# Kernel optimization log

Hardware: AMD Instinct MI355X
Metric: run time of the kernel (lower is better)

Reference implementation:

```python
import jax, jax.numpy as jnp
import numpy as np

T_SEG = 8      # n_segment
K_SIZE = 3     # dynamic temporal kernel size
BN_EPS = 1e-5


def setup_inputs() -> dict:
    key = jax.random.key(0)
    ks = jax.random.split(key, 8)
    B, T, C, H, W = 8, T_SEG, 256, 56, 56
    ch = C // 4          # c_hidden (reduction=4)
    th = T * 2           # t_hidden (temporal_expand=2)
    K = K_SIZE
    f32 = jnp.float32
    return {
        "x": jax.random.normal(ks[0], (B * T, C, H, W), f32),
        "w_spatial": jax.random.normal(ks[1], (1, 2, 7, 7), f32) * 0.05,   # Conv2d(2,1,7)
        "w_reduce": jax.random.normal(ks[2], (ch, C, 3, 1, 1), f32) * 0.02, # Conv3d(C,ch,(3,1,1))
        "bn_gamma": jnp.ones((ch,), f32),
        "bn_beta": jnp.zeros((ch,), f32),
        "bn_mean": jnp.zeros((ch,), f32),
        "bn_var": jnp.ones((ch,), f32),
        "w_expand": jax.random.normal(ks[3], (C, ch, 1, 1, 1), f32) * 0.02, # Conv3d(ch,C,1)
        "w_fc1": jax.random.normal(ks[4], (th, T), f32) * 0.1,
        "b_fc1": jnp.zeros((th,), f32),
        "w_fc2": jax.random.normal(ks[5], (K, th), f32) * 0.1,
        "b_fc2": jnp.zeros((K,), f32).at[K // 2].set(5.0),
    }


def reference(x, w_spatial, w_reduce, bn_gamma, bn_beta, bn_mean, bn_var,
              w_expand, w_fc1, b_fc1, w_fc2, b_fc2):
    T, K = T_SEG, K_SIZE
    BT, C, H, W = x.shape
    B = BT // T

    # ---- spatial SE gate: channel max/mean -> 7x7 conv -> sigmoid ----
    max_c = x.max(axis=1, keepdims=True)                       # (BT,1,H,W)
    avg_c = x.mean(axis=1, keepdims=True)                      # (BT,1,H,W)
    s = jax.lax.conv_general_dilated(
        jnp.concatenate([max_c, avg_c], axis=1), w_spatial,
        window_strides=(1, 1), padding=((3, 3), (3, 3)),
        dimension_numbers=("NCHW", "OIHW", "NCHW"))
    x_s = x * (1.0 + jax.nn.sigmoid(s))                        # (BT,C,H,W)

    # ---- temporal SE gate: conv3d(3,1,1) -> BN -> relu -> 1x1x1 -> sigmoid ----
    x5 = x_s.reshape(B, T, C, H, W).transpose(0, 2, 1, 3, 4)   # (B,C,T,H,W)
    t = jax.lax.conv_general_dilated(
        x5, w_reduce, window_strides=(1, 1, 1),
        padding=((1, 1), (0, 0), (0, 0)),
        dimension_numbers=("NCDHW", "OIDHW", "NCDHW"))         # (B,ch,T,H,W)
    inv = bn_gamma / jnp.sqrt(bn_var + BN_EPS)
    t = jax.nn.relu(t * inv[None, :, None, None, None]
                    + (bn_beta - bn_mean * inv)[None, :, None, None, None])
    t_attn = jax.nn.sigmoid(
        jnp.einsum("oc,bcthw->bothw", w_expand[:, :, 0, 0, 0], t))
    x_t = x5 * (1.0 + t_attn)                                  # (B,C,T,H,W)

    # ---- dynamic per-(batch,channel) temporal kernel ----
    v = x_t.mean(axis=(-2, -1))                                # (B,C,T)
    h = jax.nn.relu(jnp.einsum("bct,ht->bch", v, w_fc1) + b_fc1)
    kernel = jax.nn.softmax(jnp.einsum("bch,kh->bck", h, w_fc2) + b_fc2,
                            axis=-1)                           # (B,C,K)

    # depthwise temporal stencil (groups=B*C conv2d in torch)
    pad = K // 2
    xp = jnp.pad(x_t, ((0, 0), (0, 0), (pad, pad), (0, 0), (0, 0)))
    out = sum(kernel[:, :, k, None, None, None] * xp[:, :, k:k + T]
              for k in range(K))                               # (B,C,T,H,W)

    return out.transpose(0, 2, 1, 3, 4).reshape(BT, C, H, W)
```

## Files before the change

### kernel.cpp

```cpp
#include <hip/hip_runtime.h>
#include <stdint.h>

#define HW 3136
#define Wd 56
#define Cc 256
#define CH 64
#define Tt 8
#define Bb 8
#define VP 49

typedef unsigned short ushort_t;
typedef __attribute__((ext_vector_type(2))) unsigned short us2;
typedef __attribute__((ext_vector_type(4))) unsigned short us4;
typedef __attribute__((ext_vector_type(8))) unsigned short us8;
typedef __attribute__((ext_vector_type(8))) short short8;
typedef __attribute__((ext_vector_type(4))) float f4;
typedef __attribute__((ext_vector_type(2))) float f2;

__device__ __forceinline__ float bf2f(ushort_t u) {
    union { unsigned int i; float f; } v;
    v.i = ((unsigned int)u) << 16;
    return v.f;
}
__device__ __forceinline__ ushort_t f2bf(float f) {
    union { float f; unsigned int i; } v;
    v.f = f;
    unsigned int r = (v.i + 0x7FFFu + ((v.i >> 16) & 1u)) >> 16;
    return (ushort_t)r;
}

__global__ __launch_bounds__(256) void k0_pack(
    const float* __restrict__ wr, const float* __restrict__ bng,
    const float* __restrict__ bnb, const float* __restrict__ bnm,
    const float* __restrict__ bnv, const float* __restrict__ we,
    ushort_t* __restrict__ wpack, ushort_t* __restrict__ wepack,
    float* __restrict__ shb) {
    int bx = blockIdx.x, tid = threadIdx.x;
    if (bx < 24) {
        int dt = bx >> 3, cb = bx & 7;
        int mt = tid >> 6, l = tid & 63;
        int o = mt * 16 + (l & 15);
        float inv = bng[o] * rsqrtf(bnv[o] + 1e-5f);
        int c0 = cb * 32 + (l >> 4) * 8;
        us8 v;
#pragma unroll
        for (int j = 0; j < 8; j++)
            v[j] = f2bf(wr[((long)o * Cc + c0 + j) * 3 + dt] * inv);
        *(us8*)(wpack + (long)bx * 2048 + (mt * 64 + l) * 8) = v;
        if (bx == 0 && tid < CH)
            shb[tid] = bnb[tid] - bnm[tid] * (bng[tid] * rsqrtf(bnv[tid] + 1e-5f));
    } else {
        int u = (bx - 24) * 256 + tid;
        int l = u & 63;
        int c = ((u >> 6) & 15) * 16 + (l & 15);
        int o0 = (u >> 10) * 32 + (l >> 4) * 8;
        us8 v;
#pragma unroll
        for (int j = 0; j < 8; j++)
            v[j] = f2bf(we[(long)c * CH + o0 + j]);
        *(us8*)(wepack + (long)u * 8) = v;
    }
}

__global__ __launch_bounds__(256) void k1_pool(const float* __restrict__ x,
                                               float* __restrict__ pooledp) {
    int u = blockIdx.x * 256 + threadIdx.x;
    int q = blockIdx.y;
    int px4 = u % 784, bt = u / 784;
    long base = ((long)bt * Cc + (long)q * 64) * HW + px4 * 4;
    float mx[4], sm[4];
#pragma unroll
    for (int j = 0; j < 4; j++) { mx[j] = -3.4e38f; sm[j] = 0.f; }
    for (int c = 0; c < 64; c++) {
        f4 xv = *(const f4*)(x + base + (long)c * HW);
#pragma unroll
        for (int j = 0; j < 4; j++) {
            mx[j] = fmaxf(mx[j], xv[j]);
            sm[j] += xv[j];
        }
    }
    f4 pm, ps;
#pragma unroll
    for (int j = 0; j < 4; j++) { pm[j] = mx[j]; ps[j] = sm[j]; }
    *(f4*)(pooledp + ((long)(q * 64 + bt) * 2 + 0) * HW + px4 * 4) = pm;
    *(f4*)(pooledp + ((long)(q * 64 + bt) * 2 + 1) * HW + px4 * 4) = ps;
}

__global__ __launch_bounds__(256) void k2_conv(const float* __restrict__ pooledp,
                                               const float* __restrict__ wsp,
                                               float* __restrict__ gate) {
    __shared__ float img[2 * HW];
    __shared__ float wf[98];
    int bt = blockIdx.x, tid = threadIdx.x;
    for (int i = tid; i < HW; i += 256) {
        float m = -3.4e38f, s = 0.f;
#pragma unroll
        for (int q = 0; q < 4; q++) {
            const float* pq = pooledp + (long)(q * 64 + bt) * 2 * HW;
            m = fmaxf(m, pq[i]);
            s += pq[HW + i];
        }
        img[i] = m;
        img[HW + i] = s * (1.f / 256.f);
    }
    if (tid < 98) wf[tid] = wsp[tid];
    __syncthreads();
    for (int p = tid; p < HW; p += 256) {
        int y = p / Wd, xx = p % Wd;
        float acc = 0.f;
        for (int ci = 0; ci < 2; ci++)
            for (int ky = 0; ky < 7; ky++) {
                int yy = y + ky - 3;
                if (yy < 0 || yy >= Wd) continue;
                for (int kx = 0; kx < 7; kx++) {
                    int xc = xx + kx - 3;
                    if (xc < 0 || xc >= Wd) continue;
                    acc += wf[ci * 49 + ky * 7 + kx] * img[ci * HW + yy * Wd + xc];
                }
            }
        gate[(long)bt * HW + p] = 1.f + 1.f / (1.f + __expf(-acc));
    }
}

__global__ __launch_bounds__(512) void k23_fused(
    const float* __restrict__ x, const float* __restrict__ gate,
    const ushort_t* __restrict__ wpack, const float* __restrict__ shb,
    ushort_t* __restrict__ trelu) {
    extern __shared__ char smem[];
    ushort_t* xs = (ushort_t*)smem;
    float* gl = (float*)(smem + 256 * 72 * 2);
    int tid = threadIdx.x;
    int px0 = blockIdx.x * 32, b = blockIdx.y;
    if (tid < 256) {
        int tg = tid >> 5, pg = tid & 31;
        gl[tid] = gate[(long)(b * 8 + tg) * HW + px0 + pg];
    }
    int t = tid >> 6;
    int l = tid & 63;
    int lr = l & 15, lg = l >> 4;
    int cst = tid >> 3;
    int p4 = tid & 7;
    f4 acc[4][2];
#pragma unroll
    for (int mt = 0; mt < 4; mt++) {
        f4 bias = *(const f4*)(shb + mt * 16 + lg * 4);
        acc[mt][0] = bias;
        acc[mt][1] = bias;
    }
    __syncthreads();
    for (int ch = 0; ch < 4; ch++) {
#pragma unroll
        for (int tt = 0; tt < 8; tt++) {
            f4 xv = *(const f4*)(x + ((long)(b * 8 + tt) * Cc + ch * 64 + cst) * HW
                                 + px0 + p4 * 4);
            const float* gp = gl + tt * 32 + p4 * 4;
#pragma unroll
            for (int k = 0; k < 4; k++) {
                int p = p4 * 4 + k;
                xs[(tt * 32 + p) * 72 + (cst ^ (((p >> 3) & 7) * 8))] = f2bf(xv[k] * gp[k]);
            }
        }
        __syncthreads();
#pragma unroll
        for (int dt = 0; dt < 3; dt++) {
            int tp = t + dt - 1;
            if (tp >= 0 && tp < Tt) {
                const ushort_t* Ap = wpack + ((long)(dt * 8 + ch * 2)) * 2048 + l * 8;
#pragma unroll
                for (int kb = 0; kb < 2; kb++) {
                    short8 av[4];
#pragma unroll
                    for (int mt = 0; mt < 4; mt++)
                        av[mt] = *(const short8*)(Ap + kb * 2048 + mt * 512);
#pragma unroll
                    for (int nt = 0; nt < 2; nt++) {
                        int pxl = nt * 16 + lr;
                        short8 bv = *(const short8*)(&xs[(tp * 32 + pxl) * 72 +
                                        ((kb * 32 + lg * 8) ^ (((pxl >> 3) & 7) * 8))]);
#pragma unroll
                        for (int mt = 0; mt < 4; mt++)
                            acc[mt][nt] = __builtin_amdgcn_mfma_f32_16x16x32_bf16(
                                av[mt], bv, acc[mt][nt], 0, 0, 0);
                    }
                }
            }
        }
        __syncthreads();
    }
#pragma unroll
    for (int nt = 0; nt < 2; nt++) {
#pragma unroll
        for (int mt = 0; mt < 4; mt++) {
            us4 st;
#pragma unroll
            for (int r = 0; r < 4; r++)
                st[r] = f2bf(fmaxf(acc[mt][nt][r], 0.f));
            *(us4*)(trelu + ((long)(b * 8 + t) * HW + px0 + nt * 16 + lr) * 64
                    + mt * 16 + lg * 4) = st;
        }
    }
}

__global__ __launch_bounds__(256) void k4m(
    const float* __restrict__ x, const float* __restrict__ gate,
    const ushort_t* __restrict__ trelu, const ushort_t* __restrict__ wepack,
    ushort_t* __restrict__ xt, float* __restrict__ vpart) {
    int l = threadIdx.x, wv = threadIdx.y;
    int bt = blockIdx.y, b = bt >> 3, t = bt & 7;
    int P0 = blockIdx.x * 64;
    int lr = l & 15, lg = l >> 4;
    int ntg0 = blockIdx.z * 8 + wv * 2;

    short8 bfr[2][2];
#pragma unroll
    for (int kb = 0; kb < 2; kb++)
#pragma unroll
        for (int ni = 0; ni < 2; ni++)
            bfr[kb][ni] = *(const short8*)(wepack + ((long)(kb * 16 + ntg0 + ni) * 64 + l) * 8);

    f4 acc[4][2];
#pragma unroll
    for (int mi = 0; mi < 4; mi++)
#pragma unroll
        for (int ni = 0; ni < 2; ni++) acc[mi][ni] = f4{0.f, 0.f, 0.f, 0.f};

    const ushort_t* Ab = trelu + ((long)bt * HW + P0 + lr) * 64;
#pragma unroll
    for (int mi = 0; mi < 4; mi++) {
#pragma unroll
        for (int kb = 0; kb < 2; kb++) {
            short8 av = *(const short8*)(Ab + (long)mi * 16 * 64 + kb * 32 + lg * 8);
#pragma unroll
            for (int ni = 0; ni < 2; ni++)
                acc[mi][ni] = __builtin_amdgcn_mfma_f32_16x16x32_bf16(av, bfr[kb][ni],
                                                                      acc[mi][ni], 0, 0, 0);
        }
    }

    float csum[2] = {0.f, 0.f};
#pragma unroll
    for (int mi = 0; mi < 4; mi++) {
        int pxb = P0 + mi * 16 + lg * 4;
        f4 gv = *(const f4*)(gate + (long)bt * HW + pxb);
#pragma unroll
        for (int ni = 0; ni < 2; ni++) {
            int c = (ntg0 + ni) * 16 + lr;
            f4 xv = *(const f4*)(x + ((long)bt * Cc + c) * HW + pxb);
            us4 st;
            float s = 0.f;
#pragma unroll
            for (int r = 0; r < 4; r++) {
                float attn = 1.f / (1.f + __expf(-acc[mi][ni][r]));
                float v = xv[r] * gv[r] * (1.f + attn);
                st[r] = f2bf(v);
                s += v;
            }
            *(us4*)(xt + ((long)(b * Cc + c) * Tt + t) * HW + pxb) = st;
            csum[ni] += s;
        }
    }

#pragma unroll
    for (int ni = 0; ni < 2; ni++) {
        float s = csum[ni];
        s += __shfl_xor(s, 16);
        s += __shfl_xor(s, 32);
        if (lg == 0) {
            int c = (ntg0 + ni) * 16 + lr;
            vpart[((long)(b * Cc + c) * Tt + t) * VP + blockIdx.x] = s;
        }
    }
}

__global__ __launch_bounds__(256) void k5_dyn(
    const float* __restrict__ vpart, const float* __restrict__ wfc1,
    const float* __restrict__ bfc1, const float* __restrict__ wfc2,
    const float* __restrict__ bfc2, float* __restrict__ dk) {
    int u = blockIdx.x * 256 + threadIdx.x;
    int b = u >> 8, c = u & 255;
    float v[8];
#pragma unroll
    for (int t = 0; t < 8; t++) {
        float s = 0.f;
        for (int i = 0; i < VP; i++)
            s += vpart[((long)(b * Cc + c) * Tt + t) * VP + i];
        v[t] = s * (1.f / 3136.f);
    }
    float h[16];
#pragma unroll
    for (int j = 0; j < 16; j++) {
        float s = bfc1[j];
        for (int t = 0; t < 8; t++) s += wfc1[j * 8 + t] * v[t];
        h[j] = fmaxf(s, 0.f);
    }
    float l[3];
#pragma unroll
    for (int k = 0; k < 3; k++) {
        float s = bfc2[k];
        for (int j = 0; j < 16; j++) s += wfc2[k * 16 + j] * h[j];
        l[k] = s;
    }
    float m = fmaxf(l[0], fmaxf(l[1], l[2]));
    float e0 = __expf(l[0] - m), e1 = __expf(l[1] - m), e2 = __expf(l[2] - m);
    float inv = 1.f / (e0 + e1 + e2);
    dk[(long)u * 3 + 0] = e0 * inv;
    dk[(long)u * 3 + 1] = e1 * inv;
    dk[(long)u * 3 + 2] = e2 * inv;
}

__global__ __launch_bounds__(256) void k6_stencil(
    const ushort_t* __restrict__ xt, const float* __restrict__ dk,
    float* __restrict__ out) {
    int u = blockIdx.x * 256 + threadIdx.x;
    int px8 = u % 392, bc = u / 392;
    int px = px8 * 8;
    const float* kk = dk + (long)bc * 3;
    float k0 = kk[0], k1 = kk[1], k2 = kk[2];
    float pa[Tt][8];
    const ushort_t* src = xt + (long)bc * Tt * HW + px;
#pragma unroll
    for (int t = 0; t < Tt; t++) {
        us8 xv = *(const us8*)(src + (long)t * HW);
#pragma unroll
        for (int j = 0; j < 8; j++) pa[t][j] = bf2f(xv[j]);
    }
    int c = bc & 255, b = bc >> 8;
#pragma unroll
    for (int t = 0; t < Tt; t++) {
        f4 r0, r1;
#pragma unroll
        for (int j = 0; j < 4; j++) {
            float m = (t > 0) ? pa[t - 1][j] : 0.f;
            float p = (t < 7) ? pa[t + 1][j] : 0.f;
            r0[j] = k0 * m + k1 * pa[t][j] + k2 * p;
        }
#pragma unroll
        for (int j = 0; j < 4; j++) {
            float m = (t > 0) ? pa[t - 1][4 + j] : 0.f;
            float p = (t < 7) ? pa[t + 1][4 + j] : 0.f;
            r1[j] = k0 * m + k1 * pa[t][4 + j] + k2 * p;
        }
        float* op = out + ((long)(b * Tt + t) * Cc + c) * HW + px;
        *(f4*)(op) = r0;
        *(f4*)(op + 4) = r1;
    }
}

extern "C" void kernel_launch(void* const* d_in, const int* in_sizes, int n_in,
                              void* d_out, int out_size, void* d_ws, size_t ws_size,
                              hipStream_t stream) {
    const float* x    = (const float*)d_in[0];
    const float* wsp  = (const float*)d_in[1];
    const float* wr   = (const float*)d_in[2];
    const float* bng  = (const float*)d_in[3];
    const float* bnb  = (const float*)d_in[4];
    const float* bnm  = (const float*)d_in[5];
    const float* bnv  = (const float*)d_in[6];
    const float* we   = (const float*)d_in[7];
    const float* wfc1 = (const float*)d_in[8];
    const float* bfc1 = (const float*)d_in[9];
    const float* wfc2 = (const float*)d_in[10];
    const float* bfc2 = (const float*)d_in[11];
    float* out = (float*)d_out;

    char* ws = (char*)d_ws;
    size_t off = 0;
    ushort_t* trelu = (ushort_t*)(ws + off); off += (size_t)Bb * CH * Tt * HW * 2;
    float* pooledp = (float*)trelu;
    float* gate   = (float*)(ws + off); off += (size_t)64 * HW * 4;
    ushort_t* xt  = (ushort_t*)(ws + off); off += (size_t)Bb * Cc * Tt * HW * 2;
    float* vpart  = (float*)(ws + off); off += (size_t)Bb * Cc * Tt * VP * 4;
    float* dk     = (float*)(ws + off); off += (size_t)Bb * Cc * 3 * 4;
    ushort_t* wpack = (ushort_t*)(ws + off); off += (size_t)24 * 2048 * 2;
    ushort_t* wepack = (ushort_t*)(ws + off); off += (size_t)2048 * 8 * 2;
    float* shb    = (float*)(ws + off); off += (size_t)CH * 4;

    hipLaunchKernelGGL(k0_pack, dim3(32), dim3(256), 0, stream,
                       wr, bng, bnb, bnm, bnv, we, wpack, wepack, shb);
    hipLaunchKernelGGL(k1_pool, dim3(196, 4), dim3(256), 0, stream, x, pooledp);
    hipLaunchKernelGGL(k2_conv, dim3(64), dim3(256), 0, stream, pooledp, wsp, gate);
    hipLaunchKernelGGL(k23_fused, dim3(98, 8), dim3(512), 37888, stream,
                       x, gate, wpack, shb, trelu);
    hipLaunchKernelGGL(k4m, dim3(49, 64, 2), dim3(64, 4), 0, stream,
                       x, gate, trelu, wepack, xt, vpart);
    hipLaunchKernelGGL(k5_dyn, dim3(8), dim3(256), 0, stream,
                       vpart, wfc1, bfc1, wfc2, bfc2, dk);
    hipLaunchKernelGGL(k6_stencil, dim3(3136), dim3(256), 0, stream, xt, dk, out);
}
```

Before: 663.1 us.

## Split spatial conv by row bands, double-buffer k23 staging, widen k4m channel tiles

The spatial 7x7 conv kernel is split across four 14-row bands with halo rows, giving 4x more blocks for the small 64-block launch. The fused temporal-reduce kernel double-buffers its LDS staging tile so that loading the next channel chunk overlaps the MFMA work on the current one. This doubles shared memory per block, which may lower occupancy. The expand kernel drops the z-split and has each wave handle four channel tiles, so trelu A-fragments are reused more at the cost of extra registers.

```diff
diff --git a/kernel.cpp b/kernel.cpp
--- a/kernel.cpp
+++ b/kernel.cpp
@@ -89,36 +89,46 @@
 __global__ __launch_bounds__(256) void k2_conv(const float* __restrict__ pooledp,
                                                const float* __restrict__ wsp,
                                                float* __restrict__ gate) {
-    __shared__ float img[2 * HW];
+    __shared__ float img[2][20 * Wd];
     __shared__ float wf[98];
-    int bt = blockIdx.x, tid = threadIdx.x;
-    for (int i = tid; i < HW; i += 256) {
-        float m = -3.4e38f, s = 0.f;
-#pragma unroll
-        for (int q = 0; q < 4; q++) {
-            const float* pq = pooledp + (long)(q * 64 + bt) * 2 * HW;
-            m = fmaxf(m, pq[i]);
-            s += pq[HW + i];
-        }
-        img[i] = m;
-        img[HW + i] = s * (1.f / 256.f);
+    int bt = blockIdx.x, rb = blockIdx.y, tid = threadIdx.x;
+    int y0 = rb * 14;
+    for (int i = tid; i < 20 * Wd; i += 256) {
+        int ry = i / Wd, cx = i % Wd;
+        int y = y0 - 3 + ry;
+        float m = 0.f, s = 0.f;
+        if (y >= 0 && y < Wd) {
+            int p = y * Wd + cx;
+            m = -3.4e38f;
+#pragma unroll
+            for (int q = 0; q < 4; q++) {
+                const float* pq = pooledp + (long)(q * 64 + bt) * 2 * HW;
+                m = fmaxf(m, pq[p]);
+                s += pq[HW + p];
+            }
+            s *= (1.f / 256.f);
+        }
+        img[0][i] = m;
+        img[1][i] = s;
     }
     if (tid < 98) wf[tid] = wsp[tid];
     __syncthreads();
-    for (int p = tid; p < HW; p += 256) {
-        int y = p / Wd, xx = p % Wd;
+    for (int p = tid; p < 14 * Wd; p += 256) {
+        int ly = p / Wd, xx = p % Wd;
+        int y = y0 + ly;
         float acc = 0.f;
         for (int ci = 0; ci < 2; ci++)
             for (int ky = 0; ky < 7; ky++) {
                 int yy = y + ky - 3;
                 if (yy < 0 || yy >= Wd) continue;
+                int ri = yy - (y0 - 3);
                 for (int kx = 0; kx < 7; kx++) {
                     int xc = xx + kx - 3;
                     if (xc < 0 || xc >= Wd) continue;
-                    acc += wf[ci * 49 + ky * 7 + kx] * img[ci * HW + yy * Wd + xc];
+                    acc += wf[ci * 49 + ky * 7 + kx] * img[ci][ri * Wd + xc];
                 }
             }
-        gate[(long)bt * HW + p] = 1.f + 1.f / (1.f + __expf(-acc));
+        gate[(long)bt * HW + y * Wd + xx] = 1.f + 1.f / (1.f + __expf(-acc));
     }
 }
 
@@ -127,8 +137,9 @@
     const ushort_t* __restrict__ wpack, const float* __restrict__ shb,
     ushort_t* __restrict__ trelu) {
     extern __shared__ char smem[];
-    ushort_t* xs = (ushort_t*)smem;
-    float* gl = (float*)(smem + 256 * 72 * 2);
+    ushort_t* xs0 = (ushort_t*)smem;
+    ushort_t* xs1 = xs0 + 256 * 72;
+    float* gl = (float*)(smem + 2 * 256 * 72 * 2);
     int tid = threadIdx.x;
     int px0 = blockIdx.x * 32, b = blockIdx.y;
     if (tid < 256) {
@@ -147,8 +158,8 @@
         acc[mt][0] = bias;
         acc[mt][1] = bias;
     }
-    __syncthreads();
-    for (int ch = 0; ch < 4; ch++) {
+
+    auto STAGE = [&](ushort_t* buf, int ch) {
 #pragma unroll
         for (int tt = 0; tt < 8; tt++) {
             f4 xv = *(const f4*)(x + ((long)(b * 8 + tt) * Cc + ch * 64 + cst) * HW
@@ -157,10 +168,18 @@
 #pragma unroll
             for (int k = 0; k < 4; k++) {
                 int p = p4 * 4 + k;
-                xs[(tt * 32 + p) * 72 + (cst ^ (((p >> 3) & 7) * 8))] = f2bf(xv[k] * gp[k]);
+                buf[(tt * 32 + p) * 72 + (cst ^ (((p >> 3) & 7) * 8))] = f2bf(xv[k] * gp[k]);
             }
         }
-        __syncthreads();
+    };
+
+    __syncthreads();
+    STAGE(xs0, 0);
+    __syncthreads();
+    for (int ch = 0; ch < 4; ch++) {
+        ushort_t* cur = (ch & 1) ? xs1 : xs0;
+        ushort_t* nxt = (ch & 1) ? xs0 : xs1;
+        if (ch < 3) STAGE(nxt, ch + 1);
 #pragma unroll
         for (int dt = 0; dt < 3; dt++) {
             int tp = t + dt - 1;
@@ -175,7 +194,7 @@
 #pragma unroll
                     for (int nt = 0; nt < 2; nt++) {
                         int pxl = nt * 16 + lr;
-                        short8 bv = *(const short8*)(&xs[(tp * 32 + pxl) * 72 +
+                        short8 bv = *(const short8*)(&cur[(tp * 32 + pxl) * 72 +
                                         ((kb * 32 + lg * 8) ^ (((pxl >> 3) & 7) * 8))]);
 #pragma unroll
                         for (int mt = 0; mt < 4; mt++)
@@ -209,20 +228,20 @@
     int bt = blockIdx.y, b = bt >> 3, t = bt & 7;
     int P0 = blockIdx.x * 64;
     int lr = l & 15, lg = l >> 4;
-    int ntg0 = blockIdx.z * 8 + wv * 2;
-
-    short8 bfr[2][2];
+    int ntg0 = wv * 4;
+
+    short8 bfr[2][4];
 #pragma unroll
     for (int kb = 0; kb < 2; kb++)
 #pragma unroll
-        for (int ni = 0; ni < 2; ni++)
+        for (int ni = 0; ni < 4; ni++)
             bfr[kb][ni] = *(const short8*)(wepack + ((long)(kb * 16 + ntg0 + ni) * 64 + l) * 8);
 
-    f4 acc[4][2];
+    f4 acc[4][4];
 #pragma unroll
     for (int mi = 0; mi < 4; mi++)
 #pragma unroll
-        for (int ni = 0; ni < 2; ni++) acc[mi][ni] = f4{0.f, 0.f, 0.f, 0.f};
+        for (int ni = 0; ni < 4; ni++) acc[mi][ni] = f4{0.f, 0.f, 0.f, 0.f};
 
     const ushort_t* Ab = trelu + ((long)bt * HW + P0 + lr) * 64;
 #pragma unroll
@@ -231,19 +250,19 @@
         for (int kb = 0; kb < 2; kb++) {
             short8 av = *(const short8*)(Ab + (long)mi * 16 * 64 + kb * 32 + lg * 8);
 #pragma unroll
-            for (int ni = 0; ni < 2; ni++)
+            for (int ni = 0; ni < 4; ni++)
                 acc[mi][ni] = __builtin_amdgcn_mfma_f32_16x16x32_bf16(av, bfr[kb][ni],
                                                                       acc[mi][ni], 0, 0, 0);
         }
     }
 
-    float csum[2] = {0.f, 0.f};
+    float csum[4] = {0.f, 0.f, 0.f, 0.f};
 #pragma unroll
     for (int mi = 0; mi < 4; mi++) {
         int pxb = P0 + mi * 16 + lg * 4;
         f4 gv = *(const f4*)(gate + (long)bt * HW + pxb);
 #pragma unroll
-        for (int ni = 0; ni < 2; ni++) {
+        for (int ni = 0; ni < 4; ni++) {
             int c = (ntg0 + ni) * 16 + lr;
             f4 xv = *(const f4*)(x + ((long)bt * Cc + c) * HW + pxb);
             us4 st;
@@ -261,7 +280,7 @@
     }
 
 #pragma unroll
-    for (int ni = 0; ni < 2; ni++) {
+    for (int ni = 0; ni < 4; ni++) {
         float s = csum[ni];
         s += __shfl_xor(s, 16);
         s += __shfl_xor(s, 32);
@@ -378,10 +397,10 @@
     hipLaunchKernelGGL(k0_pack, dim3(32), dim3(256), 0, stream,
                        wr, bng, bnb, bnm, bnv, we, wpack, wepack, shb);
     hipLaunchKernelGGL(k1_pool, dim3(196, 4), dim3(256), 0, stream, x, pooledp);
-    hipLaunchKernelGGL(k2_conv, dim3(64), dim3(256), 0, stream, pooledp, wsp, gate);
-    hipLaunchKernelGGL(k23_fused, dim3(98, 8), dim3(512), 37888, stream,
+    hipLaunchKernelGGL(k2_conv, dim3(64, 4), dim3(256), 0, stream, pooledp, wsp, gate);
+    hipLaunchKernelGGL(k23_fused, dim3(98, 8), dim3(512), 74752, stream,
                        x, gate, wpack, shb, trelu);
-    hipLaunchKernelGGL(k4m, dim3(49, 64, 2), dim3(64, 4), 0, stream,
+    hipLaunchKernelGGL(k4m, dim3(49, 64), dim3(64, 4), 0, stream,
                        x, gate, trelu, wepack, xt, vpart);
     hipLaunchKernelGGL(k5_dyn, dim3(8), dim3(256), 0, stream,
                        vpart, wfc1, bfc1, wfc2, bfc2, dk);
```

After: 609.4 us. 8.1% less time.
